# Optimization experiments

Measured on AMD Instinct MI355X. Metric: run time of the kernel, lower is better.

## Reference

```python
import jax, jax.numpy as jnp
import numpy as np

MIN_N = 4
MAX_N = 5
MIN_FREQ = 2 ** MIN_N  # 16
DT = 0.005
W = 1.0e6
HUBER = 0.005
N0 = 5
EPS_VAR = 1e-6


def _skew(v):
    x, y, z = v[..., 0], v[..., 1], v[..., 2]
    o = jnp.zeros_like(x)
    return jnp.stack([
        jnp.stack([o, -z, y], -1),
        jnp.stack([z, o, -x], -1),
        jnp.stack([-y, x, o], -1)], -2)


def so3_exp(phi):
    """Rodrigues formula: axis-angle (M,3) -> rotation matrices (M,3,3)."""
    a2 = jnp.sum(phi * phi, axis=-1)
    small = a2 < 1e-12
    a2s = jnp.where(small, 1.0, a2)
    a = jnp.sqrt(a2s)
    sin_t = jnp.where(small, 1.0 - a2 / 6.0, jnp.sin(a) / a)
    cos_t = jnp.where(small, 0.5 - a2 / 24.0, (1.0 - jnp.cos(a)) / a2s)
    Wm = _skew(phi)
    I = jnp.eye(3, dtype=phi.dtype)
    return I + sin_t[..., None, None] * Wm + cos_t[..., None, None] * jnp.matmul(Wm, Wm)


def so3_log(R):
    """Rotation matrices (M,3,3) -> axis-angle (M,3)."""
    tr = R[..., 0, 0] + R[..., 1, 1] + R[..., 2, 2]
    cos = jnp.clip(0.5 * (tr - 1.0), -1.0 + 1e-6, 1.0 - 1e-6)
    angle = jnp.arccos(cos)
    small = angle < 1e-6
    factor = jnp.where(small, 0.5, angle / (2.0 * jnp.sin(jnp.where(small, 1.0, angle))))
    # vee(R - R^T)
    w = jnp.stack([R[..., 2, 1] - R[..., 1, 2],
                   R[..., 0, 2] - R[..., 2, 0],
                   R[..., 1, 0] - R[..., 0, 1]], -1)
    return factor[..., None] * w


def _smooth_l1_mean(x):
    ax = jnp.abs(x)
    return jnp.mean(jnp.where(ax < 1.0, 0.5 * ax * ax, ax - 0.5))


def _f_huber(rs):
    return W * _smooth_l1_mean(rs / HUBER) * HUBER ** 2


def _pairwise(R):
    # drot[::2] @ drot[1::2]
    return jnp.matmul(R[::2], R[1::2])


def _bmtm_log(A, B):
    # SO3.log(A^T B)
    return so3_log(jnp.einsum('nij,nik->njk', A, B))


def setup_inputs() -> dict:
    key = jax.random.key(0)
    ks = jax.random.split(key, 5)
    N, T = 128, 16384
    return {
        'w_hat': jax.random.normal(ks[0], (N, T, 3), jnp.float32),
        'dw_16': jax.random.normal(ks[1], (N, T, 3), jnp.float32),
        'w_gt': jax.random.normal(ks[2], (N, T, 3), jnp.float32),
        'w_mean': jax.random.normal(ks[3], (N, T, 3), jnp.float32),
        'w_std': jax.random.uniform(ks[4], (N, T, 3), jnp.float32),
    }


def reference(w_hat, dw_16, w_gt, w_mean, w_std):
    N = dw_16.shape[0]
    # --- gyro loss ---
    drot_16 = so3_exp(dw_16[:, ::MIN_FREQ].reshape(-1, 3))
    drot_hat = so3_exp(DT * w_hat.reshape(-1, 3))
    for _ in range(MIN_N):
        drot_hat = _pairwise(drot_hat)
    rs = _bmtm_log(drot_hat, drot_16).reshape(N, -1, 3)[:, N0:]
    gyro16 = _f_huber(rs)
    gyro32 = jnp.zeros((), rs.dtype)
    for k in range(MIN_N, MAX_N):
        drot_hat = _pairwise(drot_hat)
        drot_16 = _pairwise(drot_16)
        rs = _bmtm_log(drot_hat, drot_16).reshape(N, -1, 3)[:, N0:]
        gyro32 = _f_huber(rs) / 2 ** (k - MIN_N + 1) / 2.0
    # --- gaussian NLL ---
    w_var = w_std ** 2
    w_var = jnp.where(w_var < EPS_VAR, EPS_VAR, w_var)
    gap = w_gt - w_hat
    gnll = jnp.mean((jnp.log(w_var) + (gap - w_mean) ** 2 / w_var) / 2.0)
    return gyro16 + gyro32 + gnll
```

## Files before the change

kernel.cpp:

```cpp
#include <hip/hip_runtime.h>

#define THREADS 256
#define NQUAD 524288
#define BLOCKS (NQUAD / THREADS)
#define DT 0.005f
#define INV_HUBER 200.0f

#define NELEM 6291456.0
#define CNT16 391296.0
#define CNT32 194688.0

__device__ __forceinline__ void so3_exp_small(float x, float y, float z, float R[9]) {
    float a2 = x * x + y * y + z * z;
    float st = 1.0f - a2 * (1.0f / 6.0f) * (1.0f - a2 * (1.0f / 20.0f));
    float ct = 0.5f - a2 * (1.0f / 24.0f) * (1.0f - a2 * (1.0f / 30.0f));
    R[0] = 1.0f + ct * (x * x - a2);
    R[1] = ct * (x * y) - st * z;
    R[2] = ct * (x * z) + st * y;
    R[3] = ct * (x * y) + st * z;
    R[4] = 1.0f + ct * (y * y - a2);
    R[5] = ct * (y * z) - st * x;
    R[6] = ct * (x * z) - st * y;
    R[7] = ct * (y * z) + st * x;
    R[8] = 1.0f + ct * (z * z - a2);
}

__device__ __forceinline__ void so3_exp_full(float x, float y, float z, float R[9]) {
    float a2 = x * x + y * y + z * z;
    bool sm = a2 < 1e-12f;
    float a2s = sm ? 1.0f : a2;
    float a = sqrtf(a2s);
    float s, c;
    sincosf(a, &s, &c);
    float st = sm ? (1.0f - a2 * (1.0f / 6.0f)) : (s / a);
    float ct = sm ? (0.5f - a2 * (1.0f / 24.0f)) : ((1.0f - c) / a2s);
    R[0] = 1.0f + ct * (x * x - a2);
    R[1] = ct * (x * y) - st * z;
    R[2] = ct * (x * z) + st * y;
    R[3] = ct * (x * y) + st * z;
    R[4] = 1.0f + ct * (y * y - a2);
    R[5] = ct * (y * z) - st * x;
    R[6] = ct * (x * z) - st * y;
    R[7] = ct * (y * z) + st * x;
    R[8] = 1.0f + ct * (z * z - a2);
}

__device__ __forceinline__ void mm3(const float A[9], const float B[9], float C[9]) {
#pragma unroll
    for (int i = 0; i < 3; ++i) {
        float a0 = A[3 * i], a1 = A[3 * i + 1], a2 = A[3 * i + 2];
        C[3 * i + 0] = a0 * B[0] + a1 * B[3] + a2 * B[6];
        C[3 * i + 1] = a0 * B[1] + a1 * B[4] + a2 * B[7];
        C[3 * i + 2] = a0 * B[2] + a1 * B[5] + a2 * B[8];
    }
}

__device__ __forceinline__ float huber_bmtm(const float A[9], const float B[9]) {
    float tr = 0.f, w0 = 0.f, w1 = 0.f, w2 = 0.f;
#pragma unroll
    for (int k = 0; k < 3; ++k) {
        float a0 = A[3 * k], a1 = A[3 * k + 1], a2v = A[3 * k + 2];
        float b0 = B[3 * k], b1 = B[3 * k + 1], b2v = B[3 * k + 2];
        tr += a0 * b0 + a1 * b1 + a2v * b2v;
        w0 += a2v * b1 - a1 * b2v;
        w1 += a0 * b2v - a2v * b0;
        w2 += a1 * b0 - a0 * b1;
    }
    float cs = 0.5f * (tr - 1.0f);
    cs = fminf(fmaxf(cs, -1.0f + 1e-6f), 1.0f - 1e-6f);
    float ang = acosf(cs);
    float sn = sqrtf(fmaxf(1.0f - cs * cs, 0.0f));
    float fac = ang / (2.0f * sn);
    float h = 0.0f, r;
    r = fabsf(fac * w0 * INV_HUBER); h += (r < 1.0f) ? 0.5f * r * r : (r - 0.5f);
    r = fabsf(fac * w1 * INV_HUBER); h += (r < 1.0f) ? 0.5f * r * r : (r - 0.5f);
    r = fabsf(fac * w2 * INV_HUBER); h += (r < 1.0f) ? 0.5f * r * r : (r - 0.5f);
    return h;
}

__device__ __forceinline__ float gnll4(float4 h, float4 g, float4 m, float4 s) {
    float p = 0.f;
#pragma unroll
    for (int k = 0; k < 4; ++k) {
        float hv = (&h.x)[k], gv = (&g.x)[k], mv = (&m.x)[k], sv = (&s.x)[k];
        float v = fmaxf(sv * sv, 1e-6f);
        float d = gv - hv - mv;
        float rv = __builtin_amdgcn_rcpf(v);
        rv = rv * (2.0f - v * rv);
        p += __logf(v) + d * d * rv;
    }
    return p;
}

__global__ __launch_bounds__(THREADS) void dg_loss_kernel(
    const float* __restrict__ w_hat, const float* __restrict__ dw16,
    const float* __restrict__ w_gt, const float* __restrict__ w_mean,
    const float* __restrict__ w_std, double* __restrict__ partial)
{
    const int t = blockIdx.x * THREADS + threadIdx.x;
    const int lane = threadIdx.x & 63;

    const float4* hp = (const float4*)w_hat + (size_t)t * 3;
    const float4* gp = (const float4*)w_gt + (size_t)t * 3;
    const float4* mp = (const float4*)w_mean + (size_t)t * 3;
    const float4* sp = (const float4*)w_std + (size_t)t * 3;
    const int b = t >> 2;
    float4 q4 = ((const float4*)dw16)[(size_t)b * 12];

    float4 h0 = hp[0], h1 = hp[1], h2 = hp[2];
    float4 g0 = gp[0], g1 = gp[1], g2 = gp[2];
    float4 m0 = mp[0], m1 = mp[1], m2 = mp[2];
    float4 s0 = sp[0], s1 = sp[1], s2 = sp[2];

    double lg = 0.5 * (double)(gnll4(h0, g0, m0, s0) + gnll4(h1, g1, m1, s1) + gnll4(h2, g2, m2, s2));

    float E0[9], E1[9], E2[9], E3[9], T01[9], T23[9], P[9];
    so3_exp_small(DT * h0.x, DT * h0.y, DT * h0.z, E0);
    so3_exp_small(DT * h0.w, DT * h1.x, DT * h1.y, E1);
    so3_exp_small(DT * h1.z, DT * h1.w, DT * h2.x, E2);
    so3_exp_small(DT * h2.y, DT * h2.z, DT * h2.w, E3);
    mm3(E0, E1, T01);
    mm3(E2, E3, T23);
    mm3(T01, T23, P);

#pragma unroll
    for (int s = 1; s <= 2; s <<= 1) {
        float Nb[9];
#pragma unroll
        for (int e = 0; e < 9; ++e) Nb[e] = __shfl_xor(P[e], s);
        const bool rt = (lane & s) != 0;
        float A[9], B[9], T[9];
#pragma unroll
        for (int e = 0; e < 9; ++e) { A[e] = rt ? Nb[e] : P[e]; B[e] = rt ? P[e] : Nb[e]; }
        mm3(A, B, T);
#pragma unroll
        for (int e = 0; e < 9; ++e) P[e] = T[e];
    }

    float Q[9];
    so3_exp_full(q4.x, q4.y, q4.z, Q);

    double lh16 = 0.0, lh32 = 0.0;
    if ((lane & 3) == 0 && ((b & 1023) >= 5))
        lh16 = (double)huber_bmtm(P, Q);

    float Pn[9], Qn[9];
#pragma unroll
    for (int e = 0; e < 9; ++e) {
        Pn[e] = __shfl_xor(P[e], 4);
        Qn[e] = __shfl_xor(Q[e], 4);
    }
    if ((lane & 7) == 0) {
        const int c = t >> 3;
        if ((c & 511) >= 5) {
            float P32[9], Q32[9];
            mm3(P, Pn, P32);
            mm3(Q, Qn, Q32);
            lh32 = (double)huber_bmtm(P32, Q32);
        }
    }

    double part = lg * (1.0 / NELEM) + lh16 * (25.0 / CNT16) + lh32 * (6.25 / CNT32);
    __shared__ double s_p[4];
#pragma unroll
    for (int off = 32; off > 0; off >>= 1)
        part += __shfl_down(part, off);
    const int wv = threadIdx.x >> 6;
    if (lane == 0) s_p[wv] = part;
    __syncthreads();
    if (threadIdx.x == 0)
        partial[blockIdx.x] = s_p[0] + s_p[1] + s_p[2] + s_p[3];
}

__global__ __launch_bounds__(THREADS) void finalize_kernel(
    const double* __restrict__ partial, float* __restrict__ out)
{
    double s = 0.0;
#pragma unroll
    for (int i = 0; i < BLOCKS / THREADS; ++i)
        s += partial[i * THREADS + threadIdx.x];
    __shared__ double s_p[4];
#pragma unroll
    for (int off = 32; off > 0; off >>= 1)
        s += __shfl_down(s, off);
    const int lane = threadIdx.x & 63, wv = threadIdx.x >> 6;
    if (lane == 0) s_p[wv] = s;
    __syncthreads();
    if (threadIdx.x == 0)
        out[0] = (float)(s_p[0] + s_p[1] + s_p[2] + s_p[3]);
}

extern "C" void kernel_launch(void* const* d_in, const int* in_sizes, int n_in,
                              void* d_out, int out_size, void* d_ws, size_t ws_size,
                              hipStream_t stream) {
    const float* w_hat = (const float*)d_in[0];
    const float* dw16 = (const float*)d_in[1];
    const float* w_gt = (const float*)d_in[2];
    const float* w_mean = (const float*)d_in[3];
    const float* w_std = (const float*)d_in[4];
    float* out = (float*)d_out;
    double* partial = (double*)d_ws;

    dg_loss_kernel<<<BLOCKS, THREADS, 0, stream>>>(
        w_hat, dw16, w_gt, w_mean, w_std, partial);
    finalize_kernel<<<1, THREADS, 0, stream>>>(partial, out);
}
```

Before: 146.6 us.

## Coalesce input loads via LDS restaging and use fast trig/acos approximations

Loads all four elementwise inputs with a block-strided, fully coalesced float4 pattern and restages w_hat through shared memory so each thread still gets its 12 consecutive values for the rotation chain. Replaces acosf, sincosf and divisions with a polynomial acos, fast sin/cos and hardware reciprocal. Merges the 16- and 32-scale huber evaluations into one branch-free call selected per lane. Adds a block barrier and LDS traffic, and slightly lowers numeric accuracy.

```diff
diff --git a/kernel.cpp b/kernel.cpp
--- a/kernel.cpp
+++ b/kernel.cpp
@@ -9,6 +9,23 @@
 #define NELEM 6291456.0
 #define CNT16 391296.0
 #define CNT32 194688.0
+
+__device__ __forceinline__ float rcpf(float x) {
+    return __builtin_amdgcn_rcpf(x);
+}
+
+__device__ __forceinline__ float acos_poly(float x) {
+    float ax = fabsf(x);
+    float p = fmaf(ax, -0.0012624911f, 0.0066700901f);
+    p = fmaf(ax, p, -0.0170881256f);
+    p = fmaf(ax, p, 0.0308918810f);
+    p = fmaf(ax, p, -0.0501743046f);
+    p = fmaf(ax, p, 0.0889789874f);
+    p = fmaf(ax, p, -0.2145988016f);
+    p = fmaf(ax, p, 1.5707963050f);
+    float r = sqrtf(fmaxf(1.0f - ax, 0.0f)) * p;
+    return x < 0.0f ? 3.14159265358979f - r : r;
+}
 
 __device__ __forceinline__ void so3_exp_small(float x, float y, float z, float R[9]) {
     float a2 = x * x + y * y + z * z;
@@ -30,10 +47,10 @@
     bool sm = a2 < 1e-12f;
     float a2s = sm ? 1.0f : a2;
     float a = sqrtf(a2s);
-    float s, c;
-    sincosf(a, &s, &c);
-    float st = sm ? (1.0f - a2 * (1.0f / 6.0f)) : (s / a);
-    float ct = sm ? (0.5f - a2 * (1.0f / 24.0f)) : ((1.0f - c) / a2s);
+    float s = __sinf(a);
+    float c = __cosf(a);
+    float st = sm ? (1.0f - a2 * (1.0f / 6.0f)) : (s * rcpf(a));
+    float ct = sm ? (0.5f - a2 * (1.0f / 24.0f)) : ((1.0f - c) * rcpf(a2s));
     R[0] = 1.0f + ct * (x * x - a2);
     R[1] = ct * (x * y) - st * z;
     R[2] = ct * (x * z) + st * y;
@@ -68,9 +85,9 @@
     }
     float cs = 0.5f * (tr - 1.0f);
     cs = fminf(fmaxf(cs, -1.0f + 1e-6f), 1.0f - 1e-6f);
-    float ang = acosf(cs);
+    float ang = acos_poly(cs);
     float sn = sqrtf(fmaxf(1.0f - cs * cs, 0.0f));
-    float fac = ang / (2.0f * sn);
+    float fac = ang * 0.5f * rcpf(sn);
     float h = 0.0f, r;
     r = fabsf(fac * w0 * INV_HUBER); h += (r < 1.0f) ? 0.5f * r * r : (r - 0.5f);
     r = fabsf(fac * w1 * INV_HUBER); h += (r < 1.0f) ? 0.5f * r * r : (r - 0.5f);
@@ -85,7 +102,7 @@
         float hv = (&h.x)[k], gv = (&g.x)[k], mv = (&m.x)[k], sv = (&s.x)[k];
         float v = fmaxf(sv * sv, 1e-6f);
         float d = gv - hv - mv;
-        float rv = __builtin_amdgcn_rcpf(v);
+        float rv = rcpf(v);
         rv = rv * (2.0f - v * rv);
         p += __logf(v) + d * d * rv;
     }
@@ -97,28 +114,46 @@
     const float* __restrict__ w_gt, const float* __restrict__ w_mean,
     const float* __restrict__ w_std, double* __restrict__ partial)
 {
-    const int t = blockIdx.x * THREADS + threadIdx.x;
-    const int lane = threadIdx.x & 63;
-
-    const float4* hp = (const float4*)w_hat + (size_t)t * 3;
-    const float4* gp = (const float4*)w_gt + (size_t)t * 3;
-    const float4* mp = (const float4*)w_mean + (size_t)t * 3;
-    const float4* sp = (const float4*)w_std + (size_t)t * 3;
+    const int tid = threadIdx.x;
+    const int t = blockIdx.x * THREADS + tid;
+    const int lane = tid & 63;
+
+    __shared__ float4 swh[768];
+
+    const size_t base = (size_t)blockIdx.x * 768;
+    const float4* h4 = (const float4*)w_hat;
+    const float4* g4 = (const float4*)w_gt;
+    const float4* m4 = (const float4*)w_mean;
+    const float4* s4 = (const float4*)w_std;
+    float4 H[3], G[3], M[3], S[3];
+#pragma unroll
+    for (int k = 0; k < 3; ++k) {
+        H[k] = h4[base + k * 256 + tid];
+        G[k] = g4[base + k * 256 + tid];
+        M[k] = m4[base + k * 256 + tid];
+        S[k] = s4[base + k * 256 + tid];
+    }
     const int b = t >> 2;
     float4 q4 = ((const float4*)dw16)[(size_t)b * 12];
 
-    float4 h0 = hp[0], h1 = hp[1], h2 = hp[2];
-    float4 g0 = gp[0], g1 = gp[1], g2 = gp[2];
-    float4 m0 = mp[0], m1 = mp[1], m2 = mp[2];
-    float4 s0 = sp[0], s1 = sp[1], s2 = sp[2];
-
-    double lg = 0.5 * (double)(gnll4(h0, g0, m0, s0) + gnll4(h1, g1, m1, s1) + gnll4(h2, g2, m2, s2));
+#pragma unroll
+    for (int k = 0; k < 3; ++k)
+        swh[k * 256 + tid] = H[k];
+    __syncthreads();
+
+    double lg = 0.5 * (double)(gnll4(H[0], G[0], M[0], S[0]) +
+                               gnll4(H[1], G[1], M[1], S[1]) +
+                               gnll4(H[2], G[2], M[2], S[2]));
+
+    float4 r0 = swh[tid * 3 + 0];
+    float4 r1 = swh[tid * 3 + 1];
+    float4 r2 = swh[tid * 3 + 2];
 
     float E0[9], E1[9], E2[9], E3[9], T01[9], T23[9], P[9];
-    so3_exp_small(DT * h0.x, DT * h0.y, DT * h0.z, E0);
-    so3_exp_small(DT * h0.w, DT * h1.x, DT * h1.y, E1);
-    so3_exp_small(DT * h1.z, DT * h1.w, DT * h2.x, E2);
-    so3_exp_small(DT * h2.y, DT * h2.z, DT * h2.w, E3);
+    so3_exp_small(DT * r0.x, DT * r0.y, DT * r0.z, E0);
+    so3_exp_small(DT * r0.w, DT * r1.x, DT * r1.y, E1);
+    so3_exp_small(DT * r1.z, DT * r1.w, DT * r2.x, E2);
+    so3_exp_small(DT * r2.y, DT * r2.z, DT * r2.w, E3);
     mm3(E0, E1, T01);
     mm3(E2, E3, T23);
     mm3(T01, T23, P);
@@ -140,35 +175,38 @@
     float Q[9];
     so3_exp_full(q4.x, q4.y, q4.z, Q);
 
-    double lh16 = 0.0, lh32 = 0.0;
-    if ((lane & 3) == 0 && ((b & 1023) >= 5))
-        lh16 = (double)huber_bmtm(P, Q);
-
     float Pn[9], Qn[9];
 #pragma unroll
     for (int e = 0; e < 9; ++e) {
         Pn[e] = __shfl_xor(P[e], 4);
         Qn[e] = __shfl_xor(Q[e], 4);
     }
-    if ((lane & 7) == 0) {
-        const int c = t >> 3;
-        if ((c & 511) >= 5) {
-            float P32[9], Q32[9];
-            mm3(P, Pn, P32);
-            mm3(Q, Qn, Q32);
-            lh32 = (double)huber_bmtm(P32, Q32);
-        }
-    }
+    float T1[9], T2[9];
+    mm3(P, Pn, T1);
+    mm3(Q, Qn, T2);
+    const bool role16 = (lane & 3) == 0;
+    const bool role32 = (lane & 7) == 1;
+    float A[9], B[9];
+#pragma unroll
+    for (int e = 0; e < 9; ++e) {
+        A[e] = role16 ? P[e] : T1[e];
+        B[e] = role16 ? Q[e] : T2[e];
+    }
+    float hub = huber_bmtm(A, B);
+    double lh16 = 0.0, lh32 = 0.0;
+    if (role16 && ((b & 1023) >= 5)) lh16 = (double)hub;
+    const int c = t >> 3;
+    if (role32 && ((c & 511) >= 5)) lh32 = (double)hub;
 
     double part = lg * (1.0 / NELEM) + lh16 * (25.0 / CNT16) + lh32 * (6.25 / CNT32);
     __shared__ double s_p[4];
 #pragma unroll
     for (int off = 32; off > 0; off >>= 1)
         part += __shfl_down(part, off);
-    const int wv = threadIdx.x >> 6;
+    const int wv = tid >> 6;
     if (lane == 0) s_p[wv] = part;
     __syncthreads();
-    if (threadIdx.x == 0)
+    if (tid == 0)
         partial[blockIdx.x] = s_p[0] + s_p[1] + s_p[2] + s_p[3];
 }
 
```

Measured after the change: 147.5 us. About the same (+0.6%).
